# Performance work log

Hardware: AMD Instinct MI355X
Metric: run time of the kernel (lower is better)

The kernel has to match this reference:

```python
import jax, jax.numpy as jnp
import numpy as np

D_MODEL = 768
N_HEAD = 12


def setup_inputs() -> dict:
    key = jax.random.key(0)
    k1, k2, k3, k4, k5 = jax.random.split(key, 5)
    B, T, C = 4, 2048, D_MODEL
    s = 1.0 / np.sqrt(C)
    return {
        "x": jax.random.normal(k1, (B, T, C), dtype=jnp.float32),
        "w_attn": jax.random.normal(k2, (C, 3 * C), dtype=jnp.float32) * s,
        "b_attn": jax.random.normal(k3, (3 * C,), dtype=jnp.float32) * 0.02,
        "w_proj": jax.random.normal(k4, (C, C), dtype=jnp.float32) * s,
        "b_proj": jax.random.normal(k5, (C,), dtype=jnp.float32) * 0.02,
    }


def reference(x, w_attn, b_attn, w_proj, b_proj):
    B, T, C = x.shape
    H = N_HEAD
    Dh = C // H
    qkv = x @ w_attn + b_attn                      # [B, T, 3C]
    q, k, v = jnp.split(qkv, 3, axis=-1)
    # [B, H, T, Dh]
    q = q.reshape(B, T, H, Dh).transpose(0, 2, 1, 3)
    k = k.reshape(B, T, H, Dh).transpose(0, 2, 1, 3)
    v = v.reshape(B, T, H, Dh).transpose(0, 2, 1, 3)
    att = jnp.einsum("bhqd,bhkd->bhqk", q, k) * (1.0 / np.sqrt(Dh))
    causal = jnp.tril(jnp.ones((T, T), dtype=bool))
    att = jnp.where(causal[None, None, :, :], att, -jnp.inf)
    att = jax.nn.softmax(att, axis=-1)             # dropout p=0 (eval)
    y = jnp.einsum("bhqk,bhkd->bhqd", att, v)      # [B, H, T, Dh]
    y = y.transpose(0, 2, 1, 3).reshape(B, T, C)
    return y @ w_proj + b_proj
```

## Files before the change

### kernel.cpp

```cpp
#include <hip/hip_runtime.h>
#include <stdint.h>

#define NHEAD 12
#define DH 64
#define BATCH 4
#define SEQ 2048
#define CDIM 768
#define MROWS (BATCH*SEQ)

typedef __attribute__((ext_vector_type(8))) short short8;
typedef __attribute__((ext_vector_type(4))) float floatx4;
typedef unsigned int u32;

__device__ inline unsigned short f2bf(float f) {
    union { float f; unsigned u; } v; v.f = f;
    unsigned r = v.u + 0x7FFFu + ((v.u >> 16) & 1u);
    return (unsigned short)(r >> 16);
}

__device__ __forceinline__ u32 pk_bf16(float a, float b) {
    u32 d;
    asm("v_cvt_pk_bf16_f32 %0, %1, %2" : "=v"(d) : "v"(a), "v"(b));
    return d;
}

__device__ __forceinline__ void async_cp16(const unsigned short* g, unsigned short* l) {
    __builtin_amdgcn_global_load_lds(
        (const __attribute__((address_space(1))) u32*)g,
        (__attribute__((address_space(3))) u32*)l, 16, 0, 0);
}

__global__ void convert_f32_bf16(const float* __restrict__ in,
                                 unsigned short* __restrict__ out, int n) {
    int i = (blockIdx.x * blockDim.x + threadIdx.x) * 4;
    if (i + 3 < n) {
        float4 f = *(const float4*)(in + i);
        union { unsigned short s[4]; uint2 u; } p;
        p.s[0] = f2bf(f.x); p.s[1] = f2bf(f.y);
        p.s[2] = f2bf(f.z); p.s[3] = f2bf(f.w);
        *(uint2*)(out + i) = p.u;
    }
}

__global__ __launch_bounds__(256) void transpose_conv(
    const float* __restrict__ in, unsigned short* __restrict__ out,
    int K, int N) {
    __shared__ unsigned short T[64][72];
    const int k0 = blockIdx.x * 64, n0 = blockIdx.y * 64;
    const int t = threadIdx.x;
    const int nc = t & 63, kw = t >> 6;
    for (int i = 0; i < 16; i++) {
        const int kr = kw + i * 4;
        T[nc][kr] = f2bf(in[(size_t)(k0 + kr) * N + n0 + nc]);
    }
    __syncthreads();
    const int row = t >> 2, seg = t & 3;
    uint4 a = *(const uint4*)&T[row][seg * 16];
    uint4 b2 = *(const uint4*)&T[row][seg * 16 + 8];
    unsigned short* o = &out[(size_t)(n0 + row) * K + k0 + seg * 16];
    *(uint4*)o = a;
    *(uint4*)(o + 8) = b2;
}

template<int MODE, int KD, int BMN>
__global__ __launch_bounds__(256) void gemm_bf16(
    const unsigned short* __restrict__ A,
    const unsigned short* __restrict__ BT,
    const float* __restrict__ bias,
    float* __restrict__ Cout,
    unsigned short* __restrict__ Qout,
    unsigned short* __restrict__ Kout,
    unsigned short* __restrict__ VTout,
    int Ndim)
{
    constexpr int TMN = BMN / 32;
    constexpr int CH  = BMN / 64;
    __shared__ unsigned short As[3][BMN * 32];
    __shared__ unsigned short Bs[3][BMN * 32];
    const int tid  = threadIdx.x;
    const int wave = tid >> 6;
    const int lane = tid & 63;
    const int l16  = lane & 15;
    const int quad = lane >> 4;
    const int wm = wave >> 1, wn = wave & 1;
    const int m0 = blockIdx.x * BMN;
    const int n0 = blockIdx.y * BMN;

    const int rloc = lane >> 2;
    const int gs   = (((lane & 3) ^ (rloc & 3) ^ ((rloc >> 2) & 3))) * 8;
    const int ar0  = wave * (BMN / 4) + rloc;
    const int pg   = ((quad ^ (l16 & 3) ^ ((l16 >> 2) & 3))) * 8;

    floatx4 acc[TMN][TMN];
    for (int i = 0; i < TMN; i++)
        for (int j = 0; j < TMN; j++) acc[i][j] = (floatx4)0.0f;

    constexpr int NIT = KD / 32;

    auto stageTo = [&](int s, int buf) {
        const int koff = s * 32;
        for (int ch = 0; ch < CH; ch++) {
            const int row = ar0 + ch * 16;
            async_cp16(&A[(size_t)(m0 + row) * KD + koff + gs],
                       &As[buf][(wave * CH + ch) * 512]);
            async_cp16(&BT[(size_t)(n0 + row) * KD + koff + gs],
                       &Bs[buf][(wave * CH + ch) * 512]);
        }
    };
    stageTo(0, 0);
    stageTo(1, 1);

    int buf = 0;
    for (int it = 0; it < NIT; it++) {
        if (it < NIT - 1) {
            if constexpr (BMN == 128)
                asm volatile("s_waitcnt vmcnt(4)" ::: "memory");
            else
                asm volatile("s_waitcnt vmcnt(2)" ::: "memory");
        } else {
            asm volatile("s_waitcnt vmcnt(0)" ::: "memory");
        }
        asm volatile("s_barrier" ::: "memory");
        if (it + 2 < NIT) {
            int b2 = buf + 2; if (b2 >= 3) b2 -= 3;
            stageTo(it + 2, b2);
        }
        short8 a[TMN], b[TMN];
        for (int i = 0; i < TMN; i++)
            a[i] = *(const short8*)&As[buf][(wm * (BMN / 2) + i * 16 + l16) * 32 + pg];
        for (int j = 0; j < TMN; j++)
            b[j] = *(const short8*)&Bs[buf][(wn * (BMN / 2) + j * 16 + l16) * 32 + pg];
        for (int i = 0; i < TMN; i++)
            for (int j = 0; j < TMN; j++)
                acc[i][j] = __builtin_amdgcn_mfma_f32_16x16x32_bf16(
                    a[i], b[j], acc[i][j], 0, 0, 0);
        buf++; if (buf >= 3) buf = 0;
    }

    const float QSCALE = 0.18033688011112042f;
    for (int i = 0; i < TMN; i++) {
        const int mbase = m0 + wm * (BMN / 2) + i * 16 + quad * 4;
        for (int j = 0; j < TMN; j++) {
            const int ncj  = n0 + wn * (BMN / 2) + j * 16;
            const int part = ncj / CDIM;
            const int cj   = ncj - part * CDIM;
            const int ncol = ncj + l16;
            const float bv = bias[ncol];
            const int c = cj + l16;
            const int hh = c >> 6, d = c & 63;
            for (int r = 0; r < 4; r++) {
                const int m = mbase + r;
                const float v = acc[i][j][r] + bv;
                if (MODE == 0) {
                    Cout[(size_t)m * Ndim + ncol] = v;
                } else {
                    const int b_ = m >> 11, t = m & 2047;
                    const size_t bh = (size_t)(b_ * NHEAD + hh);
                    if (part == 0)
                        Qout[(bh * SEQ + t) * DH + d] = f2bf(v * QSCALE);
                    else if (part == 1)
                        Kout[(bh * SEQ + t) * DH + d] = f2bf(v);
                    else
                        VTout[(bh * DH + d) * SEQ + t] = f2bf(v);
                }
            }
        }
    }
}

__global__ __launch_bounds__(256) void attn_kernel(
    const unsigned short* __restrict__ Q,
    const unsigned short* __restrict__ K,
    const unsigned short* __restrict__ VT,
    unsigned short* __restrict__ O)
{
    __shared__ unsigned short Kl[2][2][64 * 32];
    __shared__ unsigned short Vl[2][2][64 * 32];
    __shared__ unsigned short Pl[4][16 * 68];

    const int tid  = threadIdx.x;
    const int wave = tid >> 6;
    const int lane = tid & 63;
    const int l16  = lane & 15;
    const int quad = lane >> 4;

    const int lin = blockIdx.x;
    const int grp = lin >> 3;
    const int xs  = grp & 15;
    const int bh  = ((grp >> 4) << 3) | (lin & 7);
    const int h = bh % NHEAD, b = bh / NHEAD;

    const unsigned short* Qp = Q  + (size_t)bh * SEQ * DH;
    const unsigned short* Kp = K  + (size_t)bh * SEQ * DH;
    const unsigned short* Vp = VT + (size_t)bh * DH * SEQ;

    const int rloc = lane >> 2;
    const int gofsK = ((lane & 3) ^ (rloc & 3) ^ ((rloc >> 2) & 3)) * 8;
    const int pg = ((quad ^ (l16 & 3) ^ ((l16 >> 2) & 3))) * 8;
    const int krow = wave * 16 + rloc;

    for (int pass = 0; pass < 2; pass++) {
        const int qtile = pass == 0 ? xs : 31 - xs;
        const int qb = qtile * 64;
        const int qw = qb + wave * 16;
        const int nkt = qtile + 1;

        short8 aq[2];
        for (int c = 0; c < 2; c++)
            aq[c] = *(const short8*)&Qp[(size_t)(qw + l16) * DH + c * 32 + quad * 8];

        floatx4 accO[4];
        for (int dt = 0; dt < 4; dt++) accO[dt] = (floatx4)0.0f;
        float lp = 0.0f;

        for (int c = 0; c < 2; c++) {
            async_cp16(&Kp[(size_t)krow * DH + c * 32 + gofsK],
                       &Kl[0][c][wave * 512]);
            async_cp16(&Vp[(size_t)krow * SEQ + 0 + c * 32 + gofsK],
                       &Vl[0][c][wave * 512]);
        }

        for (int kt = 0; kt < nkt; kt++) {
            const int kb  = kt * 64;
            const int cur = kt & 1;

            asm volatile("s_waitcnt vmcnt(0)" ::: "memory");
            asm volatile("s_barrier" ::: "memory");

            if (kt + 1 < nkt) {
                const int kbn = kb + 64;
                for (int c = 0; c < 2; c++) {
                    async_cp16(&Kp[(size_t)(kbn + krow) * DH + c * 32 + gofsK],
                               &Kl[cur ^ 1][c][wave * 512]);
                    async_cp16(&Vp[(size_t)krow * SEQ + kbn + c * 32 + gofsK],
                               &Vl[cur ^ 1][c][wave * 512]);
                }
            }

            floatx4 s[4];
            for (int jn = 0; jn < 4; jn++) {
                s[jn] = (floatx4)0.0f;
                for (int c = 0; c < 2; c++) {
                    short8 bk = *(const short8*)
                        &Kl[cur][c][(jn * 16 + l16) * 32 + pg];
                    s[jn] = __builtin_amdgcn_mfma_f32_16x16x32_bf16(
                        bk, aq[c], s[jn], 0, 0, 0);
                }
            }

            if (kt == nkt - 1) {
                const int q = qw + l16;
                for (int jn = 0; jn < 4; jn++) {
                    const int key = kb + jn * 16 + quad * 4;
                    for (int r = 0; r < 4; r++)
                        if (key + r > q) s[jn][r] = -1e30f;
                }
            }

            for (int jn = 0; jn < 4; jn++)
                for (int r = 0; r < 4; r++) {
                    float p = exp2f(s[jn][r]);
                    s[jn][r] = p;
                    lp += p;
                }

            for (int jn = 0; jn < 4; jn++) {
                uint2 u;
                u.x = pk_bf16(s[jn][0], s[jn][1]);
                u.y = pk_bf16(s[jn][2], s[jn][3]);
                *(uint2*)&Pl[wave][l16 * 68 + jn * 16 + quad * 4] = u;
            }
            short8 ap[2];
            for (int c = 0; c < 2; c++) {
                union { short8 v; uint2 u2[2]; } a_;
                const int base = l16 * 68 + c * 32 + quad * 8;
                a_.u2[0] = *(const uint2*)&Pl[wave][base];
                a_.u2[1] = *(const uint2*)&Pl[wave][base + 4];
                ap[c] = a_.v;
            }

            for (int dt = 0; dt < 4; dt++)
                for (int c = 0; c < 2; c++) {
                    short8 bv = *(const short8*)
                        &Vl[cur][c][(dt * 16 + l16) * 32 + pg];
                    accO[dt] = __builtin_amdgcn_mfma_f32_16x16x32_bf16(
                        ap[c], bv, accO[dt], 0, 0, 0);
                }
        }

        float L = lp;
        L += __shfl_xor(L, 16);
        L += __shfl_xor(L, 32);
        for (int r = 0; r < 4; r++) {
            const float Lr = __shfl(L, (lane & 48) | (quad * 4 + r), 64);
            const float inv = 1.0f / Lr;
            const int t = qb + wave * 16 + quad * 4 + r;
            const size_t base = ((size_t)b * SEQ + t) * CDIM + h * DH;
            for (int dt = 0; dt < 4; dt++)
                O[base + dt * 16 + l16] = f2bf(accO[dt][r] * inv);
        }
        __syncthreads();
    }
}

extern "C" void kernel_launch(void* const* d_in, const int* in_sizes, int n_in,
                              void* d_out, int out_size, void* d_ws, size_t ws_size,
                              hipStream_t stream) {
    const float* x      = (const float*)d_in[0];
    const float* w_attn = (const float*)d_in[1];
    const float* b_attn = (const float*)d_in[2];
    const float* w_proj = (const float*)d_in[3];
    const float* b_proj = (const float*)d_in[4];
    float* out = (float*)d_out;

    unsigned short* xb   = (unsigned short*)d_ws;
    unsigned short* wta  = xb  + (size_t)MROWS * CDIM;
    unsigned short* wtp  = wta + (size_t)3 * CDIM * CDIM;
    unsigned short* qws  = wtp + (size_t)CDIM * CDIM;
    unsigned short* kws  = qws + (size_t)MROWS * CDIM;
    unsigned short* vtws = kws + (size_t)MROWS * CDIM;
    unsigned short* ob   = xb;

    const int nx = MROWS * CDIM;
    convert_f32_bf16<<<nx / 1024, 256, 0, stream>>>(x, xb, nx);
    transpose_conv<<<dim3(CDIM / 64, 3 * CDIM / 64), 256, 0, stream>>>(
        w_attn, wta, CDIM, 3 * CDIM);
    transpose_conv<<<dim3(CDIM / 64, CDIM / 64), 256, 0, stream>>>(
        w_proj, wtp, CDIM, CDIM);

    dim3 g1(MROWS / 128, (3 * CDIM) / 128);
    gemm_bf16<1, CDIM, 128><<<g1, 256, 0, stream>>>(xb, wta, b_attn, nullptr,
                                                    qws, kws, vtws, 3 * CDIM);

    attn_kernel<<<768, 256, 0, stream>>>(qws, kws, vtws, ob);

    dim3 g3(MROWS / 64, CDIM / 64);
    gemm_bf16<0, CDIM, 64><<<g3, 256, 0, stream>>>(ob, wtp, b_proj, out,
                                                   nullptr, nullptr, nullptr, CDIM);
}
```

Measured before the change: 226.2 us.

## Fuse prep kernels, stage V-transpose epilogue through LDS, widen proj GEMM tile

Merges the x conversion and both weight transposes into a single prep kernel to cut two launches. In the QKV GEMM, blocks that produce V now write a bf16 tile into shared memory and emit coalesced 16-byte rows of V^T, replacing strided scalar stores. The GEMM template gains separate BM/BN, and the output projection moves from 64x64 to 64x128 tiles, which halves its block count and raises per-block reuse at the cost of more registers and LDS.

```diff
diff --git a/kernel.cpp b/kernel.cpp
--- a/kernel.cpp
+++ b/kernel.cpp
@@ -30,23 +30,15 @@
         (__attribute__((address_space(3))) u32*)l, 16, 0, 0);
 }
 
-__global__ void convert_f32_bf16(const float* __restrict__ in,
-                                 unsigned short* __restrict__ out, int n) {
-    int i = (blockIdx.x * blockDim.x + threadIdx.x) * 4;
-    if (i + 3 < n) {
-        float4 f = *(const float4*)(in + i);
-        union { unsigned short s[4]; uint2 u; } p;
-        p.s[0] = f2bf(f.x); p.s[1] = f2bf(f.y);
-        p.s[2] = f2bf(f.z); p.s[3] = f2bf(f.w);
-        *(uint2*)(out + i) = p.u;
-    }
-}
-
-__global__ __launch_bounds__(256) void transpose_conv(
+template<int N> __device__ __forceinline__ void waitcnt_vm() {
+    if constexpr (N == 0)      asm volatile("s_waitcnt vmcnt(0)" ::: "memory");
+    else if constexpr (N == 3) asm volatile("s_waitcnt vmcnt(3)" ::: "memory");
+    else if constexpr (N == 4) asm volatile("s_waitcnt vmcnt(4)" ::: "memory");
+}
+
+__device__ __forceinline__ void transpose_tile(
     const float* __restrict__ in, unsigned short* __restrict__ out,
-    int K, int N) {
-    __shared__ unsigned short T[64][72];
-    const int k0 = blockIdx.x * 64, n0 = blockIdx.y * 64;
+    int K, int N, int k0, int n0, unsigned short (*T)[72]) {
     const int t = threadIdx.x;
     const int nc = t & 63, kw = t >> 6;
     for (int i = 0; i < 16; i++) {
@@ -62,7 +54,29 @@
     *(uint4*)(o + 8) = b2;
 }
 
-template<int MODE, int KD, int BMN>
+__global__ __launch_bounds__(256) void prep_kernel(
+    const float* __restrict__ x,      unsigned short* __restrict__ xb,
+    const float* __restrict__ wa,     unsigned short* __restrict__ wta,
+    const float* __restrict__ wp,     unsigned short* __restrict__ wtp) {
+    __shared__ unsigned short T[64][72];
+    const int lin = blockIdx.x;
+    if (lin < 6144) {
+        const int i = (lin * 256 + threadIdx.x) * 4;
+        float4 f = *(const float4*)(x + i);
+        union { unsigned short s[4]; uint2 u; } p;
+        p.s[0] = f2bf(f.x); p.s[1] = f2bf(f.y);
+        p.s[2] = f2bf(f.z); p.s[3] = f2bf(f.w);
+        *(uint2*)(xb + i) = p.u;
+    } else if (lin < 6144 + 432) {
+        const int t2 = lin - 6144;
+        transpose_tile(wa, wta, CDIM, 3 * CDIM, (t2 % 12) * 64, (t2 / 12) * 64, T);
+    } else {
+        const int t3 = lin - 6576;
+        transpose_tile(wp, wtp, CDIM, CDIM, (t3 % 12) * 64, (t3 / 12) * 64, T);
+    }
+}
+
+template<int MODE, int KD, int BM, int BN>
 __global__ __launch_bounds__(256) void gemm_bf16(
     const unsigned short* __restrict__ A,
     const unsigned short* __restrict__ BT,
@@ -73,38 +87,42 @@
     unsigned short* __restrict__ VTout,
     int Ndim)
 {
-    constexpr int TMN = BMN / 32;
-    constexpr int CH  = BMN / 64;
-    __shared__ unsigned short As[3][BMN * 32];
-    __shared__ unsigned short Bs[3][BMN * 32];
+    constexpr int TM = BM / 32, TN = BN / 32;
+    constexpr int CHA = BM / 64, CHB = BN / 64;
+    __shared__ unsigned short SH[3 * (BM + BN) * 32];
+    auto As = [&](int b3) { return &SH[b3 * BM * 32]; };
+    auto Bs = [&](int b3) { return &SH[3 * BM * 32 + b3 * BN * 32]; };
+
     const int tid  = threadIdx.x;
     const int wave = tid >> 6;
     const int lane = tid & 63;
     const int l16  = lane & 15;
     const int quad = lane >> 4;
     const int wm = wave >> 1, wn = wave & 1;
-    const int m0 = blockIdx.x * BMN;
-    const int n0 = blockIdx.y * BMN;
+    const int m0 = blockIdx.x * BM;
+    const int n0 = blockIdx.y * BN;
 
     const int rloc = lane >> 2;
     const int gs   = (((lane & 3) ^ (rloc & 3) ^ ((rloc >> 2) & 3))) * 8;
-    const int ar0  = wave * (BMN / 4) + rloc;
     const int pg   = ((quad ^ (l16 & 3) ^ ((l16 >> 2) & 3))) * 8;
 
-    floatx4 acc[TMN][TMN];
-    for (int i = 0; i < TMN; i++)
-        for (int j = 0; j < TMN; j++) acc[i][j] = (floatx4)0.0f;
+    floatx4 acc[TM][TN];
+    for (int i = 0; i < TM; i++)
+        for (int j = 0; j < TN; j++) acc[i][j] = (floatx4)0.0f;
 
     constexpr int NIT = KD / 32;
 
     auto stageTo = [&](int s, int buf) {
         const int koff = s * 32;
-        for (int ch = 0; ch < CH; ch++) {
-            const int row = ar0 + ch * 16;
+        for (int ch = 0; ch < CHA; ch++) {
+            const int row = wave * CHA * 16 + ch * 16 + rloc;
             async_cp16(&A[(size_t)(m0 + row) * KD + koff + gs],
-                       &As[buf][(wave * CH + ch) * 512]);
+                       &As(buf)[(wave * CHA + ch) * 512]);
+        }
+        for (int ch = 0; ch < CHB; ch++) {
+            const int row = wave * CHB * 16 + ch * 16 + rloc;
             async_cp16(&BT[(size_t)(n0 + row) * KD + koff + gs],
-                       &Bs[buf][(wave * CH + ch) * 512]);
+                       &Bs(buf)[(wave * CHB + ch) * 512]);
         }
     };
     stageTo(0, 0);
@@ -112,56 +130,75 @@
 
     int buf = 0;
     for (int it = 0; it < NIT; it++) {
-        if (it < NIT - 1) {
-            if constexpr (BMN == 128)
-                asm volatile("s_waitcnt vmcnt(4)" ::: "memory");
-            else
-                asm volatile("s_waitcnt vmcnt(2)" ::: "memory");
-        } else {
-            asm volatile("s_waitcnt vmcnt(0)" ::: "memory");
-        }
+        if (it < NIT - 1) waitcnt_vm<CHA + CHB>();
+        else              waitcnt_vm<0>();
         asm volatile("s_barrier" ::: "memory");
         if (it + 2 < NIT) {
             int b2 = buf + 2; if (b2 >= 3) b2 -= 3;
             stageTo(it + 2, b2);
         }
-        short8 a[TMN], b[TMN];
-        for (int i = 0; i < TMN; i++)
-            a[i] = *(const short8*)&As[buf][(wm * (BMN / 2) + i * 16 + l16) * 32 + pg];
-        for (int j = 0; j < TMN; j++)
-            b[j] = *(const short8*)&Bs[buf][(wn * (BMN / 2) + j * 16 + l16) * 32 + pg];
-        for (int i = 0; i < TMN; i++)
-            for (int j = 0; j < TMN; j++)
+        short8 a[TM], b[TN];
+        for (int i = 0; i < TM; i++)
+            a[i] = *(const short8*)&As(buf)[(wm * (BM / 2) + i * 16 + l16) * 32 + pg];
+        for (int j = 0; j < TN; j++)
+            b[j] = *(const short8*)&Bs(buf)[(wn * (BN / 2) + j * 16 + l16) * 32 + pg];
+        for (int i = 0; i < TM; i++)
+            for (int j = 0; j < TN; j++)
                 acc[i][j] = __builtin_amdgcn_mfma_f32_16x16x32_bf16(
                     a[i], b[j], acc[i][j], 0, 0, 0);
         buf++; if (buf >= 3) buf = 0;
     }
 
     const float QSCALE = 0.18033688011112042f;
-    for (int i = 0; i < TMN; i++) {
-        const int mbase = m0 + wm * (BMN / 2) + i * 16 + quad * 4;
-        for (int j = 0; j < TMN; j++) {
-            const int ncj  = n0 + wn * (BMN / 2) + j * 16;
-            const int part = ncj / CDIM;
-            const int cj   = ncj - part * CDIM;
+
+    if (MODE == 1 && (n0 / CDIM) == 2) {
+        __syncthreads();
+        unsigned short* scr = &SH[wave * (64 * 68)];
+        for (int i = 0; i < TM; i++) {
+            const int tl = i * 16 + quad * 4;
+            for (int j = 0; j < TN; j++) {
+                const int dl = j * 16 + l16;
+                const float bv = bias[n0 + wn * 64 + j * 16 + l16];
+                uint2 u;
+                u.x = pk_bf16(acc[i][j][0] + bv, acc[i][j][1] + bv);
+                u.y = pk_bf16(acc[i][j][2] + bv, acc[i][j][3] + bv);
+                *(uint2*)&scr[dl * 68 + tl] = u;
+            }
+        }
+        const int b_ = m0 >> 11;
+        const int tg = (m0 & 2047) + wm * 64;
+        const int h  = (n0 - 2 * CDIM + wn * 64) >> 6;
+        const size_t rowbase = ((size_t)(b_ * NHEAD + h)) * DH;
+        for (int p = 0; p < 8; p++) {
+            const int d  = p * 8 + (lane >> 3);
+            const int tc = (lane & 7) * 8;
+            uint4 v = *(const uint4*)&scr[d * 68 + tc];
+            *(uint4*)&VTout[(rowbase + d) * SEQ + tg + tc] = v;
+        }
+        return;
+    }
+
+    for (int i = 0; i < TM; i++) {
+        const int mbase = m0 + wm * (BM / 2) + i * 16 + quad * 4;
+        for (int j = 0; j < TN; j++) {
+            const int ncj  = n0 + wn * (BN / 2) + j * 16;
             const int ncol = ncj + l16;
             const float bv = bias[ncol];
-            const int c = cj + l16;
-            const int hh = c >> 6, d = c & 63;
             for (int r = 0; r < 4; r++) {
                 const int m = mbase + r;
                 const float v = acc[i][j][r] + bv;
                 if (MODE == 0) {
                     Cout[(size_t)m * Ndim + ncol] = v;
                 } else {
+                    const int part = ncj / CDIM;
+                    const int c = ncol - part * CDIM;
+                    const int hh = c >> 6, d = c & 63;
                     const int b_ = m >> 11, t = m & 2047;
                     const size_t bh = (size_t)(b_ * NHEAD + hh);
                     if (part == 0)
                         Qout[(bh * SEQ + t) * DH + d] = f2bf(v * QSCALE);
-                    else if (part == 1)
+                    else
                         Kout[(bh * SEQ + t) * DH + d] = f2bf(v);
-                    else
-                        VTout[(bh * DH + d) * SEQ + t] = f2bf(v);
                 }
             }
         }
@@ -321,20 +358,15 @@
     unsigned short* vtws = kws + (size_t)MROWS * CDIM;
     unsigned short* ob   = xb;
 
-    const int nx = MROWS * CDIM;
-    convert_f32_bf16<<<nx / 1024, 256, 0, stream>>>(x, xb, nx);
-    transpose_conv<<<dim3(CDIM / 64, 3 * CDIM / 64), 256, 0, stream>>>(
-        w_attn, wta, CDIM, 3 * CDIM);
-    transpose_conv<<<dim3(CDIM / 64, CDIM / 64), 256, 0, stream>>>(
-        w_proj, wtp, CDIM, CDIM);
+    prep_kernel<<<6720, 256, 0, stream>>>(x, xb, w_attn, wta, w_proj, wtp);
 
     dim3 g1(MROWS / 128, (3 * CDIM) / 128);
-    gemm_bf16<1, CDIM, 128><<<g1, 256, 0, stream>>>(xb, wta, b_attn, nullptr,
-                                                    qws, kws, vtws, 3 * CDIM);
+    gemm_bf16<1, CDIM, 128, 128><<<g1, 256, 0, stream>>>(
+        xb, wta, b_attn, nullptr, qws, kws, vtws, 3 * CDIM);
 
     attn_kernel<<<768, 256, 0, stream>>>(qws, kws, vtws, ob);
 
-    dim3 g3(MROWS / 64, CDIM / 64);
-    gemm_bf16<0, CDIM, 64><<<g3, 256, 0, stream>>>(ob, wtp, b_proj, out,
-                                                   nullptr, nullptr, nullptr, CDIM);
-}
+    dim3 g3(MROWS / 64, CDIM / 128);
+    gemm_bf16<0, CDIM, 64, 128><<<g3, 256, 0, stream>>>(
+        ob, wtp, b_proj, out, nullptr, nullptr, nullptr, CDIM);
+}
```

After: 210.8 us. 6.8% less time.
